# Kernel tuning notes

Measured on AMD Instinct MI355X. Metric: run time of the kernel, lower is better.

Reference implementation:

```python
import jax, jax.numpy as jnp
import numpy as np

ALPHA = 0.2  # LeakyReLU negative slope

def setup_inputs() -> dict:
    key = jax.random.key(0)
    kx, kw, kb, ka = jax.random.split(key, 4)
    B, K, D, H = 4, 256, 128, 4
    x = jax.random.normal(kx, (B, K, D), dtype=jnp.float32)
    # Per-head Linear(2D -> D): stored as (H, 2D, D), i.e. transposed torch layout (y = v @ W + b)
    W = jax.random.normal(kw, (H, 2 * D, D), dtype=jnp.float32) * (1.0 / np.sqrt(2 * D))
    lin_b = jax.random.normal(kb, (H, D), dtype=jnp.float32) * 0.01
    # Per-head attention vector a: (H, D)
    a = jax.random.normal(ka, (H, D), dtype=jnp.float32) * (1.0 / np.sqrt(D))
    # Per-head additive bias over attention logits, initialized to zeros like the torch module
    bias = jnp.zeros((H, K, K), dtype=jnp.float32)
    return {"x": x, "W": W, "lin_b": lin_b, "a": a, "bias": bias}

def reference(x, W, lin_b, a, bias):
    # GATv2, dense all-pairs attention over K nodes, eval mode (dropout off).
    # Faithful decomposition: Linear(concat(x_i, x_j)) == x_i @ W_src + x_j @ W_dst + b
    B, K, D = x.shape
    H = W.shape[0]
    outs = []
    for h in range(H):  # small fixed head count; each head has distinct params
        W_src, W_dst = W[h, :D], W[h, D:]          # (D, D) each
        left = x @ W_src                            # (B, K, D) -> contribution of node i
        right = x @ W_dst                           # (B, K, D) -> contribution of node j
        s = left[:, :, None, :] + right[:, None, :, :] + lin_b[h]  # (B, K, K, D)
        s = jnp.where(s > 0, s, ALPHA * s)          # LeakyReLU
        e = jnp.einsum('bijd,d->bij', s, a[h]) + bias[h]           # (B, K, K)
        attn = jax.nn.softmax(e, axis=2)
        outs.append(attn @ x)                       # (B, K, D)
    return jnp.mean(jnp.stack(outs, axis=-1), axis=-1)
```

## Files before the change

### kernel.cpp

```cpp
#include <hip/hip_runtime.h>
#include <math.h>

constexpr int Kc = 256, Dc = 128, Mc = 1024;

typedef _Float16 h2_t __attribute__((ext_vector_type(2)));
union U32H2 { unsigned int u; h2_t h; };
__device__ inline h2_t u2h(unsigned int u) { U32H2 x; x.u = u; return x.h; }
__device__ inline unsigned int h2u(h2_t h) { U32H2 x; x.h = h; return x.u; }
__device__ inline unsigned int packh(float a, float b) {
    h2_t h; h.x = (_Float16)a; h.y = (_Float16)b; return h2u(h);
}

#if __has_builtin(__builtin_amdgcn_fdot2)
__device__ inline float dot2h(unsigned int a, unsigned int b, float c) {
    return __builtin_amdgcn_fdot2(u2h(a), u2h(b), c, false);
}
#else
__device__ inline float dot2h(unsigned int a, unsigned int b, float c) {
    h2_t ah = u2h(a), bh = u2h(b);
    return fmaf((float)ah.x, (float)bh.x, fmaf((float)ah.y, (float)bh.y, c));
}
#endif

__device__ inline float estep(unsigned int r, unsigned int l, h2_t av, float acc) {
    h2_t s = u2h(r) + u2h(l);
    unsigned int t = h2u(s) & 0x7FFF7FFFu;
#if __has_builtin(__builtin_amdgcn_fdot2)
    return __builtin_amdgcn_fdot2(u2h(t), av, acc, false);
#else
    h2_t th = u2h(t);
    return fmaf((float)th.x, (float)av.x, fmaf((float)th.y, (float)av.y, acc));
#endif
}

__global__ __launch_bounds__(256) void k1(const float* __restrict__ x,
                                          const float* __restrict__ W,
                                          const float* __restrict__ lin_b,
                                          const float* __restrict__ a,
                                          unsigned int* __restrict__ Lpp,
                                          unsigned int* __restrict__ Rtp,
                                          float* __restrict__ eb) {
    __shared__ unsigned int As2[64 * 64];
    __shared__ unsigned int Bs2[64 * 64];
    __shared__ float red[4][16][4];

    const int tid = threadIdx.x;
    const int bid = blockIdx.x;
    const int tx = tid & 15, ty = tid >> 4;
    const bool isL = (bid < 128);

    int h, b, m0, n0, dt;
    if (isL) {
        const int nt = bid & 1, mt = (bid >> 1) & 15;
        h = (bid >> 5) & 3; b = 0; dt = 0;
        m0 = mt * 64; n0 = nt * 64;
        {
            const int m_l = tid & 63, kq = tid >> 6;
            #pragma unroll
            for (int c = 0; c < 8; ++c) {
                const float4 v = *(const float4*)&x[(m0 + m_l) * Dc + kq * 32 + c * 4];
                As2[(kq * 16 + c * 2 + 0) * 64 + m_l] = packh(v.x, v.y);
                As2[(kq * 16 + c * 2 + 1) * 64 + m_l] = packh(v.z, v.w);
            }
        }
        {
            const int n_l = tid & 63, kq = tid >> 6;
            const float* Wb = W + (h * 2) * Dc * Dc;
            #pragma unroll
            for (int kk = 0; kk < 16; ++kk) {
                const int k2 = kq * 16 + kk;
                Bs2[k2 * 64 + n_l] =
                    packh(Wb[(2 * k2) * Dc + n0 + n_l], Wb[(2 * k2 + 1) * Dc + n0 + n_l]);
            }
        }
    } else {
        const int r_ = bid - 128;
        const int jt = r_ & 3;
        dt = (r_ >> 2) & 1;
        b  = (r_ >> 3) & 3;
        h  = (r_ >> 5) & 3;
        m0 = dt * 64;
        n0 = jt * 64;
        {
            const int d_l = tid & 63, kq = tid >> 6;
            const float* Wb = W + ((h * 2 + 1) * Dc) * Dc;
            #pragma unroll
            for (int kk = 0; kk < 16; ++kk) {
                const int k2 = kq * 16 + kk;
                As2[k2 * 64 + d_l] =
                    packh(Wb[(2 * k2) * Dc + m0 + d_l], Wb[(2 * k2 + 1) * Dc + m0 + d_l]);
            }
        }
        {
            const int j_l = tid & 63, kq = tid >> 6;
            #pragma unroll
            for (int c = 0; c < 8; ++c) {
                const float4 v = *(const float4*)&x[(b * Kc + n0 + j_l) * Dc + kq * 32 + c * 4];
                Bs2[(kq * 16 + c * 2 + 0) * 64 + j_l] = packh(v.x, v.y);
                Bs2[(kq * 16 + c * 2 + 1) * 64 + j_l] = packh(v.z, v.w);
            }
        }
    }
    __syncthreads();

    float acc[4][4];
    #pragma unroll
    for (int r = 0; r < 4; ++r)
        #pragma unroll
        for (int c = 0; c < 4; ++c) acc[r][c] = 0.f;

    #pragma unroll 8
    for (int k2 = 0; k2 < 64; ++k2) {
        const uint4 xa = *(const uint4*)&As2[k2 * 64 + ty * 4];
        const uint4 wb = *(const uint4*)&Bs2[k2 * 64 + tx * 4];
        acc[0][0] = dot2h(xa.x, wb.x, acc[0][0]);
        acc[0][1] = dot2h(xa.x, wb.y, acc[0][1]);
        acc[0][2] = dot2h(xa.x, wb.z, acc[0][2]);
        acc[0][3] = dot2h(xa.x, wb.w, acc[0][3]);
        acc[1][0] = dot2h(xa.y, wb.x, acc[1][0]);
        acc[1][1] = dot2h(xa.y, wb.y, acc[1][1]);
        acc[1][2] = dot2h(xa.y, wb.z, acc[1][2]);
        acc[1][3] = dot2h(xa.y, wb.w, acc[1][3]);
        acc[2][0] = dot2h(xa.z, wb.x, acc[2][0]);
        acc[2][1] = dot2h(xa.z, wb.y, acc[2][1]);
        acc[2][2] = dot2h(xa.z, wb.z, acc[2][2]);
        acc[2][3] = dot2h(xa.z, wb.w, acc[2][3]);
        acc[3][0] = dot2h(xa.w, wb.x, acc[3][0]);
        acc[3][1] = dot2h(xa.w, wb.y, acc[3][1]);
        acc[3][2] = dot2h(xa.w, wb.z, acc[3][2]);
        acc[3][3] = dot2h(xa.w, wb.w, acc[3][3]);
    }

    if (isL) {
        const float4 lv = *(const float4*)&lin_b[h * Dc + n0 + tx * 4];
        #pragma unroll
        for (int r = 0; r < 4; ++r) {
            uint2 pk;
            pk.x = packh(acc[r][0] + lv.x, acc[r][1] + lv.y);
            pk.y = packh(acc[r][2] + lv.z, acc[r][3] + lv.w);
            *(uint2*)&Lpp[(h * Mc + m0 + ty * 4 + r) * 64 + (n0 >> 1) + tx * 2] = pk;
        }
    } else {
        #pragma unroll
        for (int rp = 0; rp < 2; ++rp) {
            uint4 pk;
            pk.x = packh(acc[2 * rp][0], acc[2 * rp + 1][0]);
            pk.y = packh(acc[2 * rp][1], acc[2 * rp + 1][1]);
            pk.z = packh(acc[2 * rp][2], acc[2 * rp + 1][2]);
            pk.w = packh(acc[2 * rp][3], acc[2 * rp + 1][3]);
            *(uint4*)&Rtp[((h * 4 + b) * 64 + (m0 >> 1) + ty * 2 + rp) * Kc + n0 + tx * 4] = pk;
        }
        const float4 av = *(const float4*)&a[h * Dc + m0 + ty * 4];
        float p0 = 0.4f * (av.x * acc[0][0] + av.y * acc[1][0] + av.z * acc[2][0] + av.w * acc[3][0]);
        float p1 = 0.4f * (av.x * acc[0][1] + av.y * acc[1][1] + av.z * acc[2][1] + av.w * acc[3][1]);
        float p2 = 0.4f * (av.x * acc[0][2] + av.y * acc[1][2] + av.z * acc[2][2] + av.w * acc[3][2]);
        float p3 = 0.4f * (av.x * acc[0][3] + av.y * acc[1][3] + av.z * acc[2][3] + av.w * acc[3][3]);
        p0 += __shfl_xor(p0, 16, 64); p0 += __shfl_xor(p0, 32, 64);
        p1 += __shfl_xor(p1, 16, 64); p1 += __shfl_xor(p1, 32, 64);
        p2 += __shfl_xor(p2, 16, 64); p2 += __shfl_xor(p2, 32, 64);
        p3 += __shfl_xor(p3, 16, 64); p3 += __shfl_xor(p3, 32, 64);
        if (((tid >> 4) & 3) == 0) {
            const int w = tid >> 6;
            red[w][tx][0] = p0; red[w][tx][1] = p1;
            red[w][tx][2] = p2; red[w][tx][3] = p3;
        }
        __syncthreads();
        if (tid < 64) {
            const int txl = tid >> 2, c = tid & 3;
            const float v = red[0][txl][c] + red[1][txl][c] + red[2][txl][c] + red[3][txl][c];
            eb[((h * 4 + b) * 2 + dt) * Kc + n0 + tid] = 1.5f * v;
        }
    }
}

#define E4(ACC, LPV)                               \
    ACC.x = estep(rr.x, LPV, av, ACC.x);           \
    ACC.y = estep(rr.y, LPV, av, ACC.y);           \
    ACC.z = estep(rr.z, LPV, av, ACC.z);           \
    ACC.w = estep(rr.w, LPV, av, ACC.w);

__global__ __launch_bounds__(256) void k2(const float* __restrict__ x,
                                          const float* __restrict__ a,
                                          const float* __restrict__ bias,
                                          const unsigned int* __restrict__ Lpp,
                                          const unsigned int* __restrict__ Rtp,
                                          const float* __restrict__ eb,
                                          float* __restrict__ out) {
    __shared__ float red[256 * 12];
    __shared__ unsigned int lpT2[4 * 64 * 2];
    __shared__ unsigned int aa2s[4 * 64];
    __shared__ float plbar[2 * Kc];

    const int tid = threadIdx.x;
    const int L = blockIdx.x;
    const int xcd = L & 7;
    const int b = xcd >> 1;
    const int it = ((L >> 3) << 1) | (xcd & 1);
    const int i0 = it * 2;

    {
        const int hs = tid >> 6, dp = tid & 63;
        uint2 v;
        v.x = Lpp[(hs * Mc + b * Kc + i0 + 0) * 64 + dp];
        v.y = Lpp[(hs * Mc + b * Kc + i0 + 1) * 64 + dp];
        *(uint2*)&lpT2[(hs * 64 + dp) * 2] = v;
        aa2s[tid] = packh(0.4f * a[hs * Dc + 2 * dp], 0.4f * a[hs * Dc + 2 * dp + 1]);
    }
    __syncthreads();

    const int h = tid >> 6, j4 = tid & 63;
    const int hb = h * 4 + b;

    float4 acc0 = make_float4(0.f, 0.f, 0.f, 0.f);
    float4 acc1 = make_float4(0.f, 0.f, 0.f, 0.f);
    {
        const unsigned int* rb = Rtp + (hb * 64) * Kc + j4 * 4;
        const unsigned int* lt = lpT2 + (h * 64) * 2;
        const unsigned int* at = aa2s + h * 64;
        #pragma unroll 8
        for (int dp = 0; dp < 64; ++dp) {
            const uint4 rr = *(const uint4*)(rb + dp * Kc);
            const uint2 lp2 = *(const uint2*)(lt + dp * 2);
            const h2_t av = u2h(at[dp]);
            E4(acc0, lp2.x);
            E4(acc1, lp2.y);
        }
    }

    {
        float4 ebs;
        {
            const float4 v0 = *(const float4*)&eb[(hb * 2 + 0) * Kc + j4 * 4];
            const float4 v1 = *(const float4*)&eb[(hb * 2 + 1) * Kc + j4 * 4];
            ebs.x = v0.x + v1.x; ebs.y = v0.y + v1.y;
            ebs.z = v0.z + v1.z; ebs.w = v0.w + v1.w;
        }
        const float4 bv0 = *(const float4*)&bias[(h * Kc + i0 + 0) * Kc + j4 * 4];
        const float4 bv1 = *(const float4*)&bias[(h * Kc + i0 + 1) * Kc + j4 * 4];
        acc0.x += ebs.x + bv0.x; acc0.y += ebs.y + bv0.y;
        acc0.z += ebs.z + bv0.z; acc0.w += ebs.w + bv0.w;
        acc1.x += ebs.x + bv1.x; acc1.y += ebs.y + bv1.y;
        acc1.z += ebs.z + bv1.z; acc1.w += ebs.w + bv1.w;

        {
            float m = fmaxf(fmaxf(acc0.x, acc0.y), fmaxf(acc0.z, acc0.w));
            #pragma unroll
            for (int off = 1; off < 64; off <<= 1) m = fmaxf(m, __shfl_xor(m, off, 64));
            const float p0 = __expf(acc0.x - m), p1 = __expf(acc0.y - m);
            const float p2 = __expf(acc0.z - m), p3 = __expf(acc0.w - m);
            float s = p0 + p1 + p2 + p3;
            #pragma unroll
            for (int off = 1; off < 64; off <<= 1) s += __shfl_xor(s, off, 64);
            const float sc = 0.25f / s;
            *(float4*)&red[h * 512 + 0 * Kc + j4 * 4] =
                make_float4(p0 * sc, p1 * sc, p2 * sc, p3 * sc);
        }
        {
            float m = fmaxf(fmaxf(acc1.x, acc1.y), fmaxf(acc1.z, acc1.w));
            #pragma unroll
            for (int off = 1; off < 64; off <<= 1) m = fmaxf(m, __shfl_xor(m, off, 64));
            const float p0 = __expf(acc1.x - m), p1 = __expf(acc1.y - m);
            const float p2 = __expf(acc1.z - m), p3 = __expf(acc1.w - m);
            float s = p0 + p1 + p2 + p3;
            #pragma unroll
            for (int off = 1; off < 64; off <<= 1) s += __shfl_xor(s, off, 64);
            const float sc = 0.25f / s;
            *(float4*)&red[h * 512 + 1 * Kc + j4 * 4] =
                make_float4(p0 * sc, p1 * sc, p2 * sc, p3 * sc);
        }
    }
    __syncthreads();

    if (tid < 128) {
        const int r = tid >> 6, c = tid & 63;
        float4 s = make_float4(0.f, 0.f, 0.f, 0.f);
        #pragma unroll
        for (int w4 = 0; w4 < 4; ++w4) {
            const float4 v = *(const float4*)&red[w4 * 512 + r * Kc + c * 4];
            s.x += v.x; s.y += v.y; s.z += v.z; s.w += v.w;
        }
        *(float4*)&plbar[r * Kc + c * 4] = s;
    }
    __syncthreads();

    const int jq = tid >> 5, dd4 = tid & 31;
    float4 o0 = make_float4(0.f, 0.f, 0.f, 0.f);
    float4 o1 = make_float4(0.f, 0.f, 0.f, 0.f);
    {
        const float* xb = x + (b * Kc) * Dc + dd4 * 4;
        #pragma unroll 4
        for (int jj = 0; jj < 32; ++jj) {
            const int j = jj * 8 + jq;
            const float4 xv = *(const float4*)(xb + j * Dc);
            const float pv0 = plbar[j];
            const float pv1 = plbar[Kc + j];
            o0.x = fmaf(pv0, xv.x, o0.x); o0.y = fmaf(pv0, xv.y, o0.y);
            o0.z = fmaf(pv0, xv.z, o0.z); o0.w = fmaf(pv0, xv.w, o0.w);
            o1.x = fmaf(pv1, xv.x, o1.x); o1.y = fmaf(pv1, xv.y, o1.y);
            o1.z = fmaf(pv1, xv.z, o1.z); o1.w = fmaf(pv1, xv.w, o1.w);
        }
    }
    {
        float* myred = red + (jq * 32 + dd4) * 12;
        *(float4*)&myred[0] = o0;
        *(float4*)&myred[4] = o1;
    }
    __syncthreads();
    if (tid < 64) {
        const int i_f = tid >> 5, dd_f = tid & 31;
        float4 s = make_float4(0.f, 0.f, 0.f, 0.f);
        #pragma unroll
        for (int q = 0; q < 8; ++q) {
            const float4 v = *(const float4*)&red[(q * 32 + dd_f) * 12 + i_f * 4];
            s.x += v.x; s.y += v.y; s.z += v.z; s.w += v.w;
        }
        *(float4*)&out[(b * Kc + i0 + i_f) * Dc + dd_f * 4] = s;
    }
}

extern "C" void kernel_launch(void* const* d_in, const int* in_sizes, int n_in,
                              void* d_out, int out_size, void* d_ws, size_t ws_size,
                              hipStream_t stream) {
    const float* x     = (const float*)d_in[0];
    const float* W     = (const float*)d_in[1];
    const float* lin_b = (const float*)d_in[2];
    const float* a     = (const float*)d_in[3];
    const float* bias  = (const float*)d_in[4];
    float* out = (float*)d_out;

    unsigned int*   Lpp = (unsigned int*)d_ws;
    unsigned int*   Rtp = Lpp + 4 * Mc * 64;
    float*          eb  = (float*)(Rtp + 16 * 64 * Kc);

    k1<<<256, 256, 0, stream>>>(x, W, lin_b, a, Lpp, Rtp, eb);
    k2<<<512, 256, 0, stream>>>(x, a, bias, Lpp, Rtp, eb, out);
}
```

Baseline: 23.53 us.

## Double k2 block size, splitting each head's key range across two wavefronts

Kernel k2 now runs 512 threads per block. Each head uses two wavefronts that each cover half of the 256 keys with two columns per lane, where before one wavefront covered all keys with four columns per lane. Softmax max and sum reductions now combine the two waves through shared memory, which adds two block-wide barriers. The output accumulation is split over 16 row groups instead of 8. The goal is more parallelism per block to hide latency in the fp16 dot-product loop, at the cost of extra synchronisation and shared memory that may reduce occupancy.

```diff
diff --git a/kernel.cpp b/kernel.cpp
--- a/kernel.cpp
+++ b/kernel.cpp
@@ -173,23 +173,20 @@
     }
 }
 
-#define E4(ACC, LPV)                               \
-    ACC.x = estep(rr.x, LPV, av, ACC.x);           \
-    ACC.y = estep(rr.y, LPV, av, ACC.y);           \
-    ACC.z = estep(rr.z, LPV, av, ACC.z);           \
-    ACC.w = estep(rr.w, LPV, av, ACC.w);
-
-__global__ __launch_bounds__(256) void k2(const float* __restrict__ x,
+__global__ __launch_bounds__(512) void k2(const float* __restrict__ x,
                                           const float* __restrict__ a,
                                           const float* __restrict__ bias,
                                           const unsigned int* __restrict__ Lpp,
                                           const unsigned int* __restrict__ Rtp,
                                           const float* __restrict__ eb,
                                           float* __restrict__ out) {
-    __shared__ float red[256 * 12];
+    __shared__ float red[512 * 12];
     __shared__ unsigned int lpT2[4 * 64 * 2];
     __shared__ unsigned int aa2s[4 * 64];
+    __shared__ float pP[8 * Kc];
     __shared__ float plbar[2 * Kc];
+    __shared__ float smx[8][2];
+    __shared__ float ssm[8][2];
 
     const int tid = threadIdx.x;
     const int L = blockIdx.x;
@@ -198,7 +195,7 @@
     const int it = ((L >> 3) << 1) | (xcd & 1);
     const int i0 = it * 2;
 
-    {
+    if (tid < 256) {
         const int hs = tid >> 6, dp = tid & 63;
         uint2 v;
         v.x = Lpp[(hs * Mc + b * Kc + i0 + 0) * 64 + dp];
@@ -208,66 +205,66 @@
     }
     __syncthreads();
 
-    const int h = tid >> 6, j4 = tid & 63;
+    const int w = tid >> 6;
+    const int h = w >> 1, jh = w & 1, l = tid & 63;
     const int hb = h * 4 + b;
-
-    float4 acc0 = make_float4(0.f, 0.f, 0.f, 0.f);
-    float4 acc1 = make_float4(0.f, 0.f, 0.f, 0.f);
-    {
-        const unsigned int* rb = Rtp + (hb * 64) * Kc + j4 * 4;
+    const int jb = jh * 128 + l * 2;
+
+    const float2 ebs0 = *(const float2*)&eb[(hb * 2 + 0) * Kc + jb];
+    const float2 ebs1 = *(const float2*)&eb[(hb * 2 + 1) * Kc + jb];
+    const float2 bv0  = *(const float2*)&bias[(h * Kc + i0 + 0) * Kc + jb];
+    const float2 bv1  = *(const float2*)&bias[(h * Kc + i0 + 1) * Kc + jb];
+
+    float a0x = 0.f, a0y = 0.f, a1x = 0.f, a1y = 0.f;
+    {
+        const unsigned int* rb = Rtp + (hb * 64) * Kc + jb;
         const unsigned int* lt = lpT2 + (h * 64) * 2;
         const unsigned int* at = aa2s + h * 64;
         #pragma unroll 8
         for (int dp = 0; dp < 64; ++dp) {
-            const uint4 rr = *(const uint4*)(rb + dp * Kc);
+            const uint2 rr = *(const uint2*)(rb + dp * Kc);
             const uint2 lp2 = *(const uint2*)(lt + dp * 2);
             const h2_t av = u2h(at[dp]);
-            E4(acc0, lp2.x);
-            E4(acc1, lp2.y);
-        }
-    }
-
-    {
-        float4 ebs;
-        {
-            const float4 v0 = *(const float4*)&eb[(hb * 2 + 0) * Kc + j4 * 4];
-            const float4 v1 = *(const float4*)&eb[(hb * 2 + 1) * Kc + j4 * 4];
-            ebs.x = v0.x + v1.x; ebs.y = v0.y + v1.y;
-            ebs.z = v0.z + v1.z; ebs.w = v0.w + v1.w;
-        }
-        const float4 bv0 = *(const float4*)&bias[(h * Kc + i0 + 0) * Kc + j4 * 4];
-        const float4 bv1 = *(const float4*)&bias[(h * Kc + i0 + 1) * Kc + j4 * 4];
-        acc0.x += ebs.x + bv0.x; acc0.y += ebs.y + bv0.y;
-        acc0.z += ebs.z + bv0.z; acc0.w += ebs.w + bv0.w;
-        acc1.x += ebs.x + bv1.x; acc1.y += ebs.y + bv1.y;
-        acc1.z += ebs.z + bv1.z; acc1.w += ebs.w + bv1.w;
-
-        {
-            float m = fmaxf(fmaxf(acc0.x, acc0.y), fmaxf(acc0.z, acc0.w));
-            #pragma unroll
-            for (int off = 1; off < 64; off <<= 1) m = fmaxf(m, __shfl_xor(m, off, 64));
-            const float p0 = __expf(acc0.x - m), p1 = __expf(acc0.y - m);
-            const float p2 = __expf(acc0.z - m), p3 = __expf(acc0.w - m);
-            float s = p0 + p1 + p2 + p3;
-            #pragma unroll
-            for (int off = 1; off < 64; off <<= 1) s += __shfl_xor(s, off, 64);
-            const float sc = 0.25f / s;
-            *(float4*)&red[h * 512 + 0 * Kc + j4 * 4] =
-                make_float4(p0 * sc, p1 * sc, p2 * sc, p3 * sc);
-        }
-        {
-            float m = fmaxf(fmaxf(acc1.x, acc1.y), fmaxf(acc1.z, acc1.w));
-            #pragma unroll
-            for (int off = 1; off < 64; off <<= 1) m = fmaxf(m, __shfl_xor(m, off, 64));
-            const float p0 = __expf(acc1.x - m), p1 = __expf(acc1.y - m);
-            const float p2 = __expf(acc1.z - m), p3 = __expf(acc1.w - m);
-            float s = p0 + p1 + p2 + p3;
-            #pragma unroll
-            for (int off = 1; off < 64; off <<= 1) s += __shfl_xor(s, off, 64);
-            const float sc = 0.25f / s;
-            *(float4*)&red[h * 512 + 1 * Kc + j4 * 4] =
-                make_float4(p0 * sc, p1 * sc, p2 * sc, p3 * sc);
-        }
+            a0x = estep(rr.x, lp2.x, av, a0x);
+            a0y = estep(rr.y, lp2.x, av, a0y);
+            a1x = estep(rr.x, lp2.y, av, a1x);
+            a1y = estep(rr.y, lp2.y, av, a1y);
+        }
+    }
+    const float e0x = a0x + ebs0.x + ebs1.x + bv0.x;
+    const float e0y = a0y + ebs0.y + ebs1.y + bv0.y;
+    const float e1x = a1x + ebs0.x + ebs1.x + bv1.x;
+    const float e1y = a1y + ebs0.y + ebs1.y + bv1.y;
+
+    {
+        float m0 = fmaxf(e0x, e0y), m1 = fmaxf(e1x, e1y);
+        #pragma unroll
+        for (int off = 1; off < 64; off <<= 1) {
+            m0 = fmaxf(m0, __shfl_xor(m0, off, 64));
+            m1 = fmaxf(m1, __shfl_xor(m1, off, 64));
+        }
+        if (l == 0) { smx[w][0] = m0; smx[w][1] = m1; }
+    }
+    __syncthreads();
+    const float M0 = fmaxf(smx[h * 2][0], smx[h * 2 + 1][0]);
+    const float M1 = fmaxf(smx[h * 2][1], smx[h * 2 + 1][1]);
+    const float p0x = __expf(e0x - M0), p0y = __expf(e0y - M0);
+    const float p1x = __expf(e1x - M1), p1y = __expf(e1y - M1);
+    {
+        float s0 = p0x + p0y, s1 = p1x + p1y;
+        #pragma unroll
+        for (int off = 1; off < 64; off <<= 1) {
+            s0 += __shfl_xor(s0, off, 64);
+            s1 += __shfl_xor(s1, off, 64);
+        }
+        if (l == 0) { ssm[w][0] = s0; ssm[w][1] = s1; }
+    }
+    __syncthreads();
+    {
+        const float sc0 = 0.25f / (ssm[h * 2][0] + ssm[h * 2 + 1][0]);
+        const float sc1 = 0.25f / (ssm[h * 2][1] + ssm[h * 2 + 1][1]);
+        *(float2*)&pP[(h * 2 + 0) * Kc + jb] = make_float2(p0x * sc0, p0y * sc0);
+        *(float2*)&pP[(h * 2 + 1) * Kc + jb] = make_float2(p1x * sc1, p1y * sc1);
     }
     __syncthreads();
 
@@ -275,8 +272,8 @@
         const int r = tid >> 6, c = tid & 63;
         float4 s = make_float4(0.f, 0.f, 0.f, 0.f);
         #pragma unroll
-        for (int w4 = 0; w4 < 4; ++w4) {
-            const float4 v = *(const float4*)&red[w4 * 512 + r * Kc + c * 4];
+        for (int h4 = 0; h4 < 4; ++h4) {
+            const float4 v = *(const float4*)&pP[(h4 * 2 + r) * Kc + c * 4];
             s.x += v.x; s.y += v.y; s.z += v.z; s.w += v.w;
         }
         *(float4*)&plbar[r * Kc + c * 4] = s;
@@ -289,8 +286,8 @@
     {
         const float* xb = x + (b * Kc) * Dc + dd4 * 4;
         #pragma unroll 4
-        for (int jj = 0; jj < 32; ++jj) {
-            const int j = jj * 8 + jq;
+        for (int jj = 0; jj < 16; ++jj) {
+            const int j = jj * 16 + jq;
             const float4 xv = *(const float4*)(xb + j * Dc);
             const float pv0 = plbar[j];
             const float pv1 = plbar[Kc + j];
@@ -310,7 +307,7 @@
         const int i_f = tid >> 5, dd_f = tid & 31;
         float4 s = make_float4(0.f, 0.f, 0.f, 0.f);
         #pragma unroll
-        for (int q = 0; q < 8; ++q) {
+        for (int q = 0; q < 16; ++q) {
             const float4 v = *(const float4*)&red[(q * 32 + dd_f) * 12 + i_f * 4];
             s.x += v.x; s.y += v.y; s.z += v.z; s.w += v.w;
         }
@@ -333,5 +330,5 @@
     float*          eb  = (float*)(Rtp + 16 * 64 * Kc);
 
     k1<<<256, 256, 0, stream>>>(x, W, lin_b, a, Lpp, Rtp, eb);
-    k2<<<512, 256, 0, stream>>>(x, a, bias, Lpp, Rtp, eb, out);
-}
+    k2<<<512, 512, 0, stream>>>(x, a, bias, Lpp, Rtp, eb, out);
+}
```

Measured after the change: 25.28 us. +7.4%, slower.
